# Optimization experiments

Hardware: AMD Instinct MI355X
Metric: run time of the kernel (lower is better)

The kernel has to match this reference:

```python
import jax, jax.numpy as jnp
import numpy as np

DIM = 1536; NH = 12; HD = DIM // NH; C = HD // 2  # C = 64
F, H, W = 12, 16, 16; S = F * H * W  # 3072 tokens
NFPB = 3       # num_frame_per_block (block-causal granularity)
LOCAL = 6      # local_attn_size in frames
SINK = 1       # sink_size in frames
EPS = 1e-06


def setup_inputs():
    key = jax.random.key(0)
    ks = jax.random.split(key, 6)
    sc = 1.0 / np.sqrt(DIM)
    x = jax.random.normal(ks[0], (1, S, DIM), jnp.float32)
    Wq = jax.random.normal(ks[1], (DIM, DIM), jnp.float32) * sc
    Wk = jax.random.normal(ks[2], (DIM, DIM), jnp.float32) * sc
    Wv = jax.random.normal(ks[3], (DIM, DIM), jnp.float32) * sc
    Wo = jax.random.normal(ks[4], (DIM, DIM), jnp.float32) * sc
    zeros = jnp.zeros((DIM,), jnp.float32); ones = jnp.ones((DIM,), jnp.float32)
    # RoPE table: unit-modulus complex freqs stored as cos/sin, shape [1024, C]
    ang = jax.random.uniform(ks[5], (1024, C), jnp.float32) * (2.0 * np.pi)
    return dict(x=x, Wq=Wq, bq=zeros, Wk=Wk, bk=zeros, Wv=Wv, bv=zeros,
                Wo=Wo, bo=zeros, gq=ones, gk=ones,
                freqs_cos=jnp.cos(ang), freqs_sin=jnp.sin(ang), f=F, h=H, w=W)


def _rms_norm(x, g):
    y = x * jax.lax.rsqrt(jnp.mean(x * x, axis=-1, keepdims=True) + EPS)
    return y * g


def _pos_table(tab, f, h, w):
    # split [1024, C] into frame/height/width parts and broadcast to [f*h*w, C]
    cf = C - 2 * (C // 3); ch = C // 3
    tf = jnp.broadcast_to(tab[:f, :cf][:, None, None, :], (f, h, w, cf))
    th = jnp.broadcast_to(tab[:h, cf:cf + ch][None, :, None, :], (f, h, w, ch))
    tw = jnp.broadcast_to(tab[:w, cf + ch:][None, None, :, :], (f, h, w, ch))
    return jnp.concatenate([tf, th, tw], axis=-1).reshape(f * h * w, C)


def _rope(x, cosp, sinp):
    # complex multiply on consecutive (real, imag) pairs along head_dim
    b, s, n, d = x.shape
    xp = x.reshape(b, s, n, d // 2, 2)
    xr, xi = xp[..., 0], xp[..., 1]
    cp = cosp[None, :, None, :]; sp = sinp[None, :, None, :]
    out = jnp.stack([xr * cp - xi * sp, xr * sp + xi * cp], axis=-1)
    return out.reshape(b, s, n, d)


def reference(x, Wq, bq, Wk, bk, Wv, bv, Wo, bo, gq, gk, freqs_cos, freqs_sin, f, h, w):
    b, s, _ = x.shape
    q = _rms_norm(x @ Wq.T + bq, gq).reshape(b, s, NH, HD)
    k = _rms_norm(x @ Wk.T + bk, gk).reshape(b, s, NH, HD)
    v = (x @ Wv.T + bv).reshape(b, s, NH, HD)
    cosp = _pos_table(freqs_cos, f, h, w)
    sinp = _pos_table(freqs_sin, f, h, w)
    rq = _rope(q, cosp, sinp)
    rk = _rope(k, cosp, sinp)
    # block mask: block-causal (bidirectional inside a frame-block) + local window + sink
    idx = jnp.arange(s)
    frame = idx // (h * w)
    blk = frame // NFPB
    qb, kb = blk[:, None], blk[None, :]
    mask = (kb <= qb) & ((((qb - kb) * NFPB) < LOCAL) | (frame[None, :] < SINK))
    scores = jnp.einsum('bqnd,bknd->bnqk', rq, rk) * (HD ** -0.5)
    scores = jnp.where(mask[None, None], scores, jnp.finfo(scores.dtype).min)
    probs = jax.nn.softmax(scores, axis=-1)
    out = jnp.einsum('bnqk,bknd->bqnd', probs, v).reshape(b, s, DIM)
    return out @ Wo.T + bo
```

## Files before the change

kernel.cpp:

```cpp
#include <hip/hip_runtime.h>
#include <stdint.h>

typedef unsigned short u16;
typedef __attribute__((ext_vector_type(8))) short bf16x8;
typedef __attribute__((ext_vector_type(4))) short bf16x4;
typedef __attribute__((ext_vector_type(4))) float f32x4;

constexpr int DMODEL = 1536;
constexpr int SEQ    = 3072;
constexpr int NHEAD  = 12;
constexpr int HDIM   = 128;

__device__ __forceinline__ u16 f2bf(float f){
  union { float f; unsigned u; } v; v.f = f;
  return (u16)((v.u + 0x7fffu + ((v.u >> 16) & 1u)) >> 16);
}

__global__ __launch_bounds__(256) void cvt_all(
    const float* __restrict__ x,  const float* __restrict__ wq,
    const float* __restrict__ wk, const float* __restrict__ wv, const float* __restrict__ wo,
    u16* __restrict__ xb, u16* __restrict__ wqb, u16* __restrict__ wkb,
    u16* __restrict__ wvb, u16* __restrict__ wob)
{
  const int NX = (SEQ * DMODEL) / 4;
  const int NW = (DMODEL * DMODEL) / 4;
  int i = blockIdx.x * 256 + threadIdx.x;
  const float* src; u16* dst; int off;
  if      (i < NX)          { src = x;  dst = xb;  off = i; }
  else if (i < NX + NW)     { src = wq; dst = wqb; off = i - NX; }
  else if (i < NX + 2 * NW) { src = wk; dst = wkb; off = i - NX - NW; }
  else if (i < NX + 3 * NW) { src = wv; dst = wvb; off = i - NX - 2 * NW; }
  else                      { src = wo; dst = wob; off = i - NX - 3 * NW; }
  float4 f = ((const float4*)src)[off];
  ushort4 o;
  o.x = f2bf(f.x); o.y = f2bf(f.y); o.z = f2bf(f.z); o.w = f2bf(f.w);
  ((ushort4*)dst)[off] = o;
}

__device__ __forceinline__ void gload16(const u16* g, u16* l){
  __builtin_amdgcn_global_load_lds((const __attribute__((address_space(1))) void*)g,
                                   (__attribute__((address_space(3))) void*)l, 16, 0, 0);
}

__global__ __launch_bounds__(512, 2) void gemm_qkv256(const u16* __restrict__ xb,
    const u16* __restrict__ wqb, const u16* __restrict__ wkb, const u16* __restrict__ wvb,
    const float* __restrict__ bq, const float* __restrict__ bk, const float* __restrict__ bv,
    float* __restrict__ qf, float* __restrict__ kf, u16* __restrict__ vt)
{
  __shared__ u16 lds[2][2][16384];

  const int tid  = threadIdx.x;
  const int lane = tid & 63;
  const int wid  = tid >> 6;
  const int wm   = wid >> 2;
  const int wn   = wid & 3;
  const int l15  = lane & 15, lg = lane >> 4;
  const int swz  = (l15 & 7) << 4;

  const int bid  = blockIdx.x;
  const int sbid = (bid & 7) * 27 + (bid >> 3);
  const int mt   = sbid / 18, nt = sbid % 18;
  const int sel  = nt / 6, ntl = nt % 6;
  const u16* W = sel == 0 ? wqb : (sel == 1 ? wkb : wvb);
  const float* bias = sel == 0 ? bq : (sel == 1 ? bk : bv);
  const int m0 = mt * 256, n0 = ntl * 256;

  const char* Ag = (const char*)(xb + (size_t)m0 * DMODEL);
  const char* Bg = (const char*)(W  + (size_t)n0 * DMODEL);

  auto stage_op = [&](int buf, int op, const char* G, int kt){
#pragma unroll
    for (int c = 0; c < 4; c++){
      int ob  = c * 8192 + wid * 1024 + lane * 16;
      int row = ob >> 7, colb = ob & 127;
      gload16((const u16*)(G + (size_t)row * (DMODEL * 2) + (size_t)kt * 128
                             + (colb ^ ((row & 7) << 4))),
              (u16*)((char*)&lds[buf][op][0] + c * 8192 + wid * 1024));
    }
  };

  f32x4 acc[8][4];
#pragma unroll
  for (int i = 0; i < 8; i++)
#pragma unroll
    for (int j = 0; j < 4; j++){ f32x4 z = {0.f,0.f,0.f,0.f}; acc[i][j] = z; }

  const int NK = DMODEL / 64;

  stage_op(0, 0, Ag, 0);
  stage_op(0, 1, Bg, 0);
  asm volatile("s_waitcnt vmcnt(0)" ::: "memory");
  __builtin_amdgcn_sched_barrier(0);
  __builtin_amdgcn_s_barrier();
  __builtin_amdgcn_sched_barrier(0);

#pragma unroll 1
  for (int t = 0; t < NK; t++){
    const int b = t & 1;
    const char* Abase = (const char*)&lds[b][0][0];
    const char* Bbase = (const char*)&lds[b][1][0];
    bf16x8 bfr[4][2], afr[2][2];

#pragma unroll
    for (int ni = 0; ni < 4; ni++){
      int rb = wn * 64 + ni * 16 + l15;
#pragma unroll
      for (int ks = 0; ks < 2; ks++)
        bfr[ni][ks] = *(const bf16x8*)(Bbase + rb * 128 + ((ks * 64 + lg * 16) ^ swz));
    }
#pragma unroll
    for (int i = 0; i < 2; i++){
      int ra = wm * 128 + i * 16 + l15;
#pragma unroll
      for (int ks = 0; ks < 2; ks++)
        afr[i][ks] = *(const bf16x8*)(Abase + ra * 128 + ((ks * 64 + lg * 16) ^ swz));
    }
    if (t + 1 < NK) stage_op(b ^ 1, 0, Ag, t + 1);
    __builtin_amdgcn_sched_barrier(0);
    __builtin_amdgcn_s_barrier();
    __builtin_amdgcn_sched_barrier(0);
    __builtin_amdgcn_s_setprio(1);
#pragma unroll
    for (int i = 0; i < 2; i++)
#pragma unroll
      for (int ni = 0; ni < 4; ni++)
#pragma unroll
        for (int ks = 0; ks < 2; ks++)
          acc[i][ni] = __builtin_amdgcn_mfma_f32_16x16x32_bf16(afr[i][ks], bfr[ni][ks], acc[i][ni], 0, 0, 0);
    __builtin_amdgcn_s_setprio(0);
    __builtin_amdgcn_sched_barrier(0);
    __builtin_amdgcn_s_barrier();
    __builtin_amdgcn_sched_barrier(0);

#pragma unroll
    for (int qd = 1; qd < 4; qd++){
#pragma unroll
      for (int i = 0; i < 2; i++){
        int ra = wm * 128 + (qd * 2 + i) * 16 + l15;
#pragma unroll
        for (int ks = 0; ks < 2; ks++)
          afr[i][ks] = *(const bf16x8*)(Abase + ra * 128 + ((ks * 64 + lg * 16) ^ swz));
      }
      if (qd == 1 && t + 1 < NK) stage_op(b ^ 1, 1, Bg, t + 1);
      __builtin_amdgcn_sched_barrier(0);
      __builtin_amdgcn_s_barrier();
      __builtin_amdgcn_sched_barrier(0);
      __builtin_amdgcn_s_setprio(1);
#pragma unroll
      for (int i = 0; i < 2; i++)
#pragma unroll
        for (int ni = 0; ni < 4; ni++)
#pragma unroll
          for (int ks = 0; ks < 2; ks++)
            acc[qd * 2 + i][ni] = __builtin_amdgcn_mfma_f32_16x16x32_bf16(afr[i][ks], bfr[ni][ks], acc[qd * 2 + i][ni], 0, 0, 0);
      __builtin_amdgcn_s_setprio(0);
      if (qd == 3) asm volatile("s_waitcnt vmcnt(0)" ::: "memory");
      __builtin_amdgcn_sched_barrier(0);
      __builtin_amdgcn_s_barrier();
      __builtin_amdgcn_sched_barrier(0);
    }
  }

  if (sel != 2){
    float* C = sel == 0 ? qf : kf;
#pragma unroll
    for (int mi = 0; mi < 8; mi++){
      int row = m0 + wm * 128 + mi * 16 + lg * 4;
#pragma unroll
      for (int ni = 0; ni < 4; ni++){
        int col = n0 + wn * 64 + ni * 16 + l15;
        float bvv = bias[col];
#pragma unroll
        for (int r = 0; r < 4; r++)
          C[(size_t)(row + r) * DMODEL + col] = acc[mi][ni][r] + bvv;
      }
    }
  } else {
#pragma unroll
    for (int mi = 0; mi < 8; mi++){
      int gbase = m0 + wm * 128 + (mi >> 1) * 32 + lg * 8 + (mi & 1) * 4;
#pragma unroll
      for (int ni = 0; ni < 4; ni++){
        int d = n0 + wn * 64 + ni * 16 + l15;
        float bvv = bias[d];
        ushort4 o;
        o.x = f2bf(acc[mi][ni][0] + bvv);
        o.y = f2bf(acc[mi][ni][1] + bvv);
        o.z = f2bf(acc[mi][ni][2] + bvv);
        o.w = f2bf(acc[mi][ni][3] + bvv);
        *(ushort4*)(vt + (size_t)d * SEQ + gbase) = o;
      }
    }
  }
}

__device__ __forceinline__ void gemm_core(const u16* __restrict__ A, const u16* __restrict__ W,
    const float* __restrict__ bias, float* __restrict__ C, int m0, int n0,
    u16* As, u16* Bs)
{
  const int tid  = threadIdx.x;
  const int lane = tid & 63;
  const int wv   = tid >> 6;
  const int wm   = wv & 1, wn = wv >> 1;
  const int l15  = lane & 15, lg = lane >> 4;

  f32x4 acc[4][4];
#pragma unroll
  for (int i = 0; i < 4; i++)
#pragma unroll
    for (int j = 0; j < 4; j++){ f32x4 z = {0.f,0.f,0.f,0.f}; acc[i][j] = z; }

  const int r0 = wv * 16 + (lane >> 2);
  const int r1 = (wv + 4) * 16 + (lane >> 2);
  const int cc = (lane & 3) * 8;
  const u16* Ab = A + (size_t)m0 * DMODEL;
  const u16* Wb = W + (size_t)n0 * DMODEL;

  auto stageg = [&](int b, int k0){
    gload16(Ab + (size_t)r0 * DMODEL + k0 + cc, As + b * 4096 + wv * 512);
    gload16(Ab + (size_t)r1 * DMODEL + k0 + cc, As + b * 4096 + (wv + 4) * 512);
    gload16(Wb + (size_t)r0 * DMODEL + k0 + cc, Bs + b * 4096 + wv * 512);
    gload16(Wb + (size_t)r1 * DMODEL + k0 + cc, Bs + b * 4096 + (wv + 4) * 512);
  };

  stageg(0, 0);
  __syncthreads();

  for (int k0 = 0; k0 < DMODEL; k0 += 32){
    int b = (k0 >> 5) & 1;
    if (k0 + 32 < DMODEL) stageg(b ^ 1, k0 + 32);

    const u16* Ar = As + b * 4096;
    const u16* Br = Bs + b * 4096;
    bf16x8 af[4], bfr[4];
#pragma unroll
    for (int mi = 0; mi < 4; mi++)
      af[mi]  = *(const bf16x8*)(Ar + (wm * 64 + mi * 16 + l15) * 32 + lg * 8);
#pragma unroll
    for (int ni = 0; ni < 4; ni++)
      bfr[ni] = *(const bf16x8*)(Br + (wn * 64 + ni * 16 + l15) * 32 + lg * 8);
#pragma unroll
    for (int mi = 0; mi < 4; mi++)
#pragma unroll
      for (int ni = 0; ni < 4; ni++)
        acc[mi][ni] = __builtin_amdgcn_mfma_f32_16x16x32_bf16(af[mi], bfr[ni], acc[mi][ni], 0, 0, 0);
    __syncthreads();
  }

#pragma unroll
  for (int mi = 0; mi < 4; mi++){
    int row = m0 + wm * 64 + mi * 16 + (lg << 2);
#pragma unroll
    for (int ni = 0; ni < 4; ni++){
      int col = n0 + wn * 64 + ni * 16 + l15;
      float bvv = bias[col];
#pragma unroll
      for (int r = 0; r < 4; r++)
        C[(size_t)(row + r) * DMODEL + col] = acc[mi][ni][r] + bvv;
    }
  }
}

__global__ __launch_bounds__(256) void gemm_o(const u16* __restrict__ ab,
    const u16* __restrict__ wob, const float* __restrict__ bo, float* __restrict__ out)
{
  __shared__ u16 As[2 * 4096], Bs[2 * 4096];
  gemm_core(ab, wob, bo, out, blockIdx.x * 128, blockIdx.y * 128, As, Bs);
}

__global__ __launch_bounds__(256) void rmsrope_kernel(
    const float* __restrict__ qin, const float* __restrict__ kin,
    const float* __restrict__ gq, const float* __restrict__ gk,
    const float* __restrict__ fcos, const float* __restrict__ fsin,
    u16* __restrict__ rq, u16* __restrict__ rk)
{
  int gw   = (blockIdx.x * 256 + threadIdx.x) >> 6;
  int lane = threadIdx.x & 63;
  int s    = gw >> 1;
  int pass = gw & 1;
  const float* in = pass ? kin : qin;
  const float* g  = pass ? gk  : gq;
  u16* outp       = pass ? rk  : rq;

  const float* row = in + (size_t)s * DMODEL + lane * 24;
  float v[24];
#pragma unroll
  for (int j = 0; j < 6; j++) *(float4*)(v + 4 * j) = ((const float4*)row)[j];

  float ss = 0.f;
#pragma unroll
  for (int j = 0; j < 24; j++) ss += v[j] * v[j];
#pragma unroll
  for (int m = 1; m < 64; m <<= 1) ss += __shfl_xor(ss, m);
  float scale = rsqrtf(ss * (1.0f / (float)DMODEL) + 1e-6f);

  float gv[24];
  const float* gp = g + lane * 24;
#pragma unroll
  for (int j = 0; j < 6; j++) *(float4*)(gv + 4 * j) = ((const float4*)gp)[j];

  int fi = s >> 8, hi2 = (s >> 4) & 15, wi = s & 15;
  u16 o[24];
#pragma unroll
  for (int jp = 0; jp < 12; jp++){
    int i  = lane * 12 + jp;
    int pi = i & 63;
    int idx = pi < 22 ? fi : (pi < 43 ? hi2 : wi);
    float cv = fcos[idx * 64 + pi];
    float sv = fsin[idx * 64 + pi];
    float xr = v[2 * jp]     * scale * gv[2 * jp];
    float xi = v[2 * jp + 1] * scale * gv[2 * jp + 1];
    o[2 * jp]     = f2bf(xr * cv - xi * sv);
    o[2 * jp + 1] = f2bf(xr * sv + xi * cv);
  }
  u16* op = outp + (size_t)s * DMODEL + lane * 24;
#pragma unroll
  for (int j = 0; j < 3; j++) *(bf16x8*)(op + 8 * j) = *(bf16x8*)(o + 8 * j);
}

__global__ __launch_bounds__(256, 2) void attn_kernel(const u16* __restrict__ rq,
    const u16* __restrict__ rk, const u16* __restrict__ vt,
    float* __restrict__ pO, float* __restrict__ pl)
{
  __shared__ u16 Ks[2][8192];
  __shared__ u16 Vs[2][8192];

  const int tid  = threadIdx.x;
  const int lane = tid & 63;
  const int wv   = tid >> 6;
  const int head = blockIdx.y;
  const int bid  = blockIdx.x;
  int qb, blk, sub;
  if      (bid < 24){ qb = 3; blk = bid >> 1;        sub = bid & 1; }
  else if (bid < 48){ qb = 2; blk = (bid - 24) >> 1; sub = bid & 1; }
  else if (bid < 72){ qb = 1; blk = (bid - 48) >> 1; sub = bid & 1; }
  else              { qb = 0; blk = bid - 72;        sub = 0; }
  const int qblk = qb * 12 + blk;
  const int q0   = qblk * 64 + wv * 16;
  const int l15  = lane & 15, lg = lane >> 4;
  const int swz  = (l15 & 7) << 4;
  const float sc = 0.08838834764831845f;

  int r1s = 0, r1e = 0, r0e = 0;
  if      (qb == 0){ r0e = 768; }
  else if (qb == 1){ r0e = 1536; }
  else if (qb == 2){ r0e = 256; r1s = 768;  r1e = 2304; }
  else             { r0e = 256; r1s = 1536; r1e = 3072; }
  const int nt0 = r0e >> 6;
  const int nt  = nt0 + ((r1e - r1s) >> 6);
  const int hl  = (qb == 0) ? nt : (nt >> 1);
  const int ts  = sub * hl, te = ts + hl;

  const char* rkB = (const char*)rk;
  const char* vtB = (const char*)vt;
  auto k0_of = [&](int t){ return t < nt0 ? t * 64 : (r1s + (t - nt0) * 64); };

  auto stage = [&](int buf, int k0){
    char* Kd = (char*)Ks[buf];
    char* Vd = (char*)Vs[buf];
#pragma unroll
    for (int c = 0; c < 4; c++){
      int o = c * 4096 + wv * 1024 + lane * 16;
      int row = o >> 8, colb = o & 255;
      gload16((const u16*)(rkB + (size_t)(k0 + row) * (DMODEL * 2) + head * (HDIM * 2)
                               + (colb ^ ((row & 7) << 4))),
              (u16*)(Kd + c * 4096 + wv * 1024));
    }
#pragma unroll
    for (int c = 0; c < 4; c++){
      int o = c * 4096 + wv * 1024 + lane * 16;
      int row = o >> 7, colb = o & 127;
      gload16((const u16*)(vtB + (size_t)(head * HDIM + row) * (SEQ * 2) + (size_t)k0 * 2
                               + (colb ^ ((row & 7) << 4))),
              (u16*)(Vd + c * 4096 + wv * 1024));
    }
  };

  bf16x8 qfr[4];
  const u16* qbase = rq + (size_t)(q0 + l15) * DMODEL + head * HDIM + lg * 8;
#pragma unroll
  for (int c = 0; c < 4; c++) qfr[c] = *(const bf16x8*)(qbase + c * 32);

  f32x4 oacc[8];
#pragma unroll
  for (int i = 0; i < 8; i++){ f32x4 z = {0.f,0.f,0.f,0.f}; oacc[i] = z; }
  float l_run = 0.f;

  stage(0, k0_of(ts));
  __syncthreads();

  for (int t = ts; t < te; t++){
    int buf = (t - ts) & 1;
    if (t + 1 < te) stage(buf ^ 1, k0_of(t + 1));

    const char* Kb = (const char*)Ks[buf];
    const char* Vb = (const char*)Vs[buf];
#pragma unroll
    for (int half = 0; half < 2; half++){
      const int kt = half * 32;
      const char* kr0 = Kb + (kt + l15) * 256;
      const char* kr1 = kr0 + 16 * 256;
      bf16x8 kf0[4], kf1[4];
#pragma unroll
      for (int c = 0; c < 4; c++){
        kf0[c] = *(const bf16x8*)(kr0 + ((lg * 16 + c * 64) ^ swz));
        kf1[c] = *(const bf16x8*)(kr1 + ((lg * 16 + c * 64) ^ swz));
      }
      f32x4 s0 = {0.f,0.f,0.f,0.f}, s1 = {0.f,0.f,0.f,0.f};
      __builtin_amdgcn_s_setprio(1);
#pragma unroll
      for (int c = 0; c < 4; c++){
        s0 = __builtin_amdgcn_mfma_f32_16x16x32_bf16(kf0[c], qfr[c], s0, 0, 0, 0);
        s1 = __builtin_amdgcn_mfma_f32_16x16x32_bf16(kf1[c], qfr[c], s1, 0, 0, 0);
      }
      __builtin_amdgcn_s_setprio(0);

      bf16x8 pf;
      float lsum = 0.f;
#pragma unroll
      for (int r = 0; r < 4; r++){
        float e0 = __expf(fmaf(s0[r], sc, -12.f));
        float e1 = __expf(fmaf(s1[r], sc, -12.f));
        lsum += e0 + e1;
        pf[r]     = (short)f2bf(e0);
        pf[r + 4] = (short)f2bf(e1);
      }
      l_run += lsum;

      __builtin_amdgcn_s_setprio(1);
#pragma unroll
      for (int ch = 0; ch < 8; ch++){
        bf16x8 vf8 = *(const bf16x8*)(Vb + (ch * 16 + l15) * 128 + ((half * 64 + lg * 16) ^ swz));
        oacc[ch] = __builtin_amdgcn_mfma_f32_16x16x32_bf16(pf, vf8, oacc[ch], 0, 0, 0);
      }
      __builtin_amdgcn_s_setprio(0);
    }
    __syncthreads();
  }

  const size_t punit = (size_t)(head * 84 + bid);
  l_run += __shfl_xor(l_run, 16);
  l_run += __shfl_xor(l_run, 32);
  if (lg == 0) pl[punit * 64 + wv * 16 + l15] = l_run;

  float* po = pO + punit * 8192;
#pragma unroll
  for (int ch = 0; ch < 8; ch++)
#pragma unroll
    for (int r = 0; r < 4; r++)
      po[(wv * 16 + lg * 4 + r) * 128 + ch * 16 + l15] = oacc[ch][r];
}

__global__ __launch_bounds__(256) void attn_reduce(const float* __restrict__ pO,
    const float* __restrict__ pl, u16* __restrict__ ao)
{
  const int qblk = blockIdx.x;
  const int head = blockIdx.y;
  const int qb = qblk / 12, blk = qblk % 12;
  int b0, nu;
  if      (qb == 0){ b0 = 72 + blk;     nu = 1; }
  else if (qb == 1){ b0 = 48 + 2 * blk; nu = 2; }
  else if (qb == 2){ b0 = 24 + 2 * blk; nu = 2; }
  else             { b0 = 2 * blk;      nu = 2; }
  const size_t u0 = (size_t)(head * 84 + b0);
  const float* O0 = pO + u0 * 8192;
  const float* L0 = pl + u0 * 64;

  __shared__ float ls[64];
  int t = threadIdx.x;
  if (t < 64) ls[t] = L0[t] + (nu == 2 ? L0[64 + t] : 0.f);
  __syncthreads();

  int q = t >> 2, dc = (t & 3) * 32;
  float inv = 1.f / ls[q];
  const float* a0 = O0 + q * 128 + dc;
  const float* a1 = a0 + 8192;
  u16 buf[32];
#pragma unroll
  for (int j = 0; j < 32; j += 4){
    float4 xv = *(const float4*)(a0 + j);
    if (nu == 2){
      float4 y = *(const float4*)(a1 + j);
      xv.x += y.x; xv.y += y.y; xv.z += y.z; xv.w += y.w;
    }
    buf[j]     = f2bf(xv.x * inv);
    buf[j + 1] = f2bf(xv.y * inv);
    buf[j + 2] = f2bf(xv.z * inv);
    buf[j + 3] = f2bf(xv.w * inv);
  }
  u16* op = ao + (size_t)(qblk * 64 + q) * DMODEL + head * HDIM + dc;
#pragma unroll
  for (int j = 0; j < 32; j += 8) *(bf16x8*)(op + j) = *(bf16x8*)(buf + j);
}

extern "C" void kernel_launch(void* const* d_in, const int* in_sizes, int n_in,
                              void* d_out, int out_size, void* d_ws, size_t ws_size,
                              hipStream_t stream)
{
  const float* x    = (const float*)d_in[0];
  const float* Wq   = (const float*)d_in[1];
  const float* bq   = (const float*)d_in[2];
  const float* Wk   = (const float*)d_in[3];
  const float* bk   = (const float*)d_in[4];
  const float* Wv   = (const float*)d_in[5];
  const float* bv   = (const float*)d_in[6];
  const float* Wo   = (const float*)d_in[7];
  const float* bo   = (const float*)d_in[8];
  const float* gq   = (const float*)d_in[9];
  const float* gk   = (const float*)d_in[10];
  const float* fcos = (const float*)d_in[11];
  const float* fsin = (const float*)d_in[12];
  float* out = (float*)d_out;

  char* ws = (char*)d_ws;
  size_t off = 0;
  auto alloc = [&](size_t bytes){
    void* p = ws + off;
    off += (bytes + 255) & ~(size_t)255;
    return p;
  };
  const size_t SD = (size_t)SEQ * DMODEL;
  const size_t WW = (size_t)DMODEL * DMODEL;
  u16*   xb  = (u16*)  alloc(SD * 2);
  u16*   wqb = (u16*)  alloc(WW * 2);
  u16*   wkb = (u16*)  alloc(WW * 2);
  u16*   wvb = (u16*)  alloc(WW * 2);
  u16*   wob = (u16*)  alloc(WW * 2);
  float* qf  = (float*)alloc(SD * 4);
  float* kf  = (float*)alloc(SD * 4);
  u16*   rq  = (u16*)  alloc(SD * 2);
  u16*   rk  = (u16*)  alloc(SD * 2);
  u16*   vt  = (u16*)  alloc(SD * 2);
  u16*   ao  = (u16*)  alloc(SD * 2);
  float* pl  = (float*)alloc((size_t)1008 * 64 * 4);
  float* pO  = qf;

  const int NX = (SEQ * DMODEL) / 4, NW = (DMODEL * DMODEL) / 4;
  cvt_all<<<(NX + 4 * NW) / 256, 256, 0, stream>>>(x, Wq, Wk, Wv, Wo, xb, wqb, wkb, wvb, wob);
  gemm_qkv256<<<216, 512, 0, stream>>>(xb, wqb, wkb, wvb, bq, bk, bv, qf, kf, vt);
  rmsrope_kernel<<<(SEQ * 2) / 4, 256, 0, stream>>>(qf, kf, gq, gk, fcos, fsin, rq, rk);
  attn_kernel<<<dim3(84, NHEAD), 256, 0, stream>>>(rq, rk, vt, pO, pl);
  attn_reduce<<<dim3(48, NHEAD), 256, 0, stream>>>(pO, pl, ao);
  gemm_o<<<dim3(SEQ / 128, DMODEL / 128), 256, 0, stream>>>(ao, wob, bo, out);
}
```

Before: 289.9 us.

## Double attention query tile to 128 rows and remap blocks for XCD locality

Each attention workgroup now handles 128 query rows instead of 64, with every wave processing two 16-row query groups that share the same K/V fragments loaded from shared memory. This halves K/V global and LDS traffic per query row. The 1D grid is remapped with a stride-8 interleave so that blocks of the same head land on the same XCD. The reduce kernel and partial-buffer layout are adjusted to match. The cost is more registers per thread (doubled accumulators) and fewer workgroups (504 vs 1008), which may reduce occupancy and load balance.

```diff
diff --git a/kernel.cpp b/kernel.cpp
--- a/kernel.cpp
+++ b/kernel.cpp
@@ -328,15 +328,17 @@
   const int tid  = threadIdx.x;
   const int lane = tid & 63;
   const int wv   = tid >> 6;
-  const int head = blockIdx.y;
-  const int bid  = blockIdx.x;
+  const int lin  = blockIdx.x;
+  const int u    = (lin & 7) * 63 + (lin >> 3);
+  const int head = u / 42;
+  const int bid  = u % 42;
   int qb, blk, sub;
-  if      (bid < 24){ qb = 3; blk = bid >> 1;        sub = bid & 1; }
-  else if (bid < 48){ qb = 2; blk = (bid - 24) >> 1; sub = bid & 1; }
-  else if (bid < 72){ qb = 1; blk = (bid - 48) >> 1; sub = bid & 1; }
-  else              { qb = 0; blk = bid - 72;        sub = 0; }
-  const int qblk = qb * 12 + blk;
-  const int q0   = qblk * 64 + wv * 16;
+  if      (bid < 12){ qb = 3; blk = bid >> 1;        sub = bid & 1; }
+  else if (bid < 24){ qb = 2; blk = (bid - 12) >> 1; sub = bid & 1; }
+  else if (bid < 36){ qb = 1; blk = (bid - 24) >> 1; sub = bid & 1; }
+  else              { qb = 0; blk = bid - 36;        sub = 0; }
+  const int qblk = qb * 6 + blk;
+  const int q0   = qblk * 128 + wv * 32;
   const int l15  = lane & 15, lg = lane >> 4;
   const int swz  = (l15 & 7) << 4;
   const float sc = 0.08838834764831845f;
@@ -376,15 +378,20 @@
     }
   };
 
-  bf16x8 qfr[4];
-  const u16* qbase = rq + (size_t)(q0 + l15) * DMODEL + head * HDIM + lg * 8;
-#pragma unroll
-  for (int c = 0; c < 4; c++) qfr[c] = *(const bf16x8*)(qbase + c * 32);
-
-  f32x4 oacc[8];
-#pragma unroll
-  for (int i = 0; i < 8; i++){ f32x4 z = {0.f,0.f,0.f,0.f}; oacc[i] = z; }
-  float l_run = 0.f;
+  bf16x8 qfr[2][4];
+#pragma unroll
+  for (int qg = 0; qg < 2; qg++){
+    const u16* qbase = rq + (size_t)(q0 + qg * 16 + l15) * DMODEL + head * HDIM + lg * 8;
+#pragma unroll
+    for (int c = 0; c < 4; c++) qfr[qg][c] = *(const bf16x8*)(qbase + c * 32);
+  }
+
+  f32x4 oacc[2][8];
+#pragma unroll
+  for (int qg = 0; qg < 2; qg++)
+#pragma unroll
+    for (int i = 0; i < 8; i++){ f32x4 z = {0.f,0.f,0.f,0.f}; oacc[qg][i] = z; }
+  float l_run[2] = {0.f, 0.f};
 
   stage(0, k0_of(ts));
   __syncthreads();
@@ -406,49 +413,64 @@
         kf0[c] = *(const bf16x8*)(kr0 + ((lg * 16 + c * 64) ^ swz));
         kf1[c] = *(const bf16x8*)(kr1 + ((lg * 16 + c * 64) ^ swz));
       }
-      f32x4 s0 = {0.f,0.f,0.f,0.f}, s1 = {0.f,0.f,0.f,0.f};
+      f32x4 s0[2], s1[2];
+#pragma unroll
+      for (int qg = 0; qg < 2; qg++){ f32x4 z = {0.f,0.f,0.f,0.f}; s0[qg] = z; s1[qg] = z; }
       __builtin_amdgcn_s_setprio(1);
 #pragma unroll
-      for (int c = 0; c < 4; c++){
-        s0 = __builtin_amdgcn_mfma_f32_16x16x32_bf16(kf0[c], qfr[c], s0, 0, 0, 0);
-        s1 = __builtin_amdgcn_mfma_f32_16x16x32_bf16(kf1[c], qfr[c], s1, 0, 0, 0);
+      for (int c = 0; c < 4; c++)
+#pragma unroll
+        for (int qg = 0; qg < 2; qg++){
+          s0[qg] = __builtin_amdgcn_mfma_f32_16x16x32_bf16(kf0[c], qfr[qg][c], s0[qg], 0, 0, 0);
+          s1[qg] = __builtin_amdgcn_mfma_f32_16x16x32_bf16(kf1[c], qfr[qg][c], s1[qg], 0, 0, 0);
+        }
+      __builtin_amdgcn_s_setprio(0);
+
+      bf16x8 pf[2];
+#pragma unroll
+      for (int qg = 0; qg < 2; qg++){
+        float lsum = 0.f;
+#pragma unroll
+        for (int r = 0; r < 4; r++){
+          float e0 = __expf(fmaf(s0[qg][r], sc, -12.f));
+          float e1 = __expf(fmaf(s1[qg][r], sc, -12.f));
+          lsum += e0 + e1;
+          pf[qg][r]     = (short)f2bf(e0);
+          pf[qg][r + 4] = (short)f2bf(e1);
+        }
+        l_run[qg] += lsum;
+      }
+
+      __builtin_amdgcn_s_setprio(1);
+#pragma unroll
+      for (int ch = 0; ch < 8; ch++){
+        bf16x8 vf8 = *(const bf16x8*)(Vb + (ch * 16 + l15) * 128 + ((half * 64 + lg * 16) ^ swz));
+#pragma unroll
+        for (int qg = 0; qg < 2; qg++)
+          oacc[qg][ch] = __builtin_amdgcn_mfma_f32_16x16x32_bf16(pf[qg], vf8, oacc[qg][ch], 0, 0, 0);
       }
       __builtin_amdgcn_s_setprio(0);
-
-      bf16x8 pf;
-      float lsum = 0.f;
-#pragma unroll
-      for (int r = 0; r < 4; r++){
-        float e0 = __expf(fmaf(s0[r], sc, -12.f));
-        float e1 = __expf(fmaf(s1[r], sc, -12.f));
-        lsum += e0 + e1;
-        pf[r]     = (short)f2bf(e0);
-        pf[r + 4] = (short)f2bf(e1);
-      }
-      l_run += lsum;
-
-      __builtin_amdgcn_s_setprio(1);
-#pragma unroll
-      for (int ch = 0; ch < 8; ch++){
-        bf16x8 vf8 = *(const bf16x8*)(Vb + (ch * 16 + l15) * 128 + ((half * 64 + lg * 16) ^ swz));
-        oacc[ch] = __builtin_amdgcn_mfma_f32_16x16x32_bf16(pf, vf8, oacc[ch], 0, 0, 0);
-      }
-      __builtin_amdgcn_s_setprio(0);
     }
     __syncthreads();
   }
 
-  const size_t punit = (size_t)(head * 84 + bid);
-  l_run += __shfl_xor(l_run, 16);
-  l_run += __shfl_xor(l_run, 32);
-  if (lg == 0) pl[punit * 64 + wv * 16 + l15] = l_run;
-
-  float* po = pO + punit * 8192;
-#pragma unroll
-  for (int ch = 0; ch < 8; ch++)
-#pragma unroll
-    for (int r = 0; r < 4; r++)
-      po[(wv * 16 + lg * 4 + r) * 128 + ch * 16 + l15] = oacc[ch][r];
+  const size_t punit = (size_t)(head * 42 + bid);
+#pragma unroll
+  for (int qg = 0; qg < 2; qg++){
+    float lr = l_run[qg];
+    lr += __shfl_xor(lr, 16);
+    lr += __shfl_xor(lr, 32);
+    if (lg == 0) pl[punit * 128 + wv * 32 + qg * 16 + l15] = lr;
+  }
+
+  float* po = pO + punit * 16384;
+#pragma unroll
+  for (int qg = 0; qg < 2; qg++)
+#pragma unroll
+    for (int ch = 0; ch < 8; ch++)
+#pragma unroll
+      for (int r = 0; r < 4; r++)
+        po[(wv * 32 + qg * 16 + lg * 4 + r) * 128 + ch * 16 + l15] = oacc[qg][ch][r];
 }
 
 __global__ __launch_bounds__(256) void attn_reduce(const float* __restrict__ pO,
@@ -456,28 +478,28 @@
 {
   const int qblk = blockIdx.x;
   const int head = blockIdx.y;
-  const int qb = qblk / 12, blk = qblk % 12;
+  const int qb = qblk / 6, blk = qblk % 6;
   int b0, nu;
-  if      (qb == 0){ b0 = 72 + blk;     nu = 1; }
-  else if (qb == 1){ b0 = 48 + 2 * blk; nu = 2; }
-  else if (qb == 2){ b0 = 24 + 2 * blk; nu = 2; }
+  if      (qb == 0){ b0 = 36 + blk;     nu = 1; }
+  else if (qb == 1){ b0 = 24 + 2 * blk; nu = 2; }
+  else if (qb == 2){ b0 = 12 + 2 * blk; nu = 2; }
   else             { b0 = 2 * blk;      nu = 2; }
-  const size_t u0 = (size_t)(head * 84 + b0);
-  const float* O0 = pO + u0 * 8192;
-  const float* L0 = pl + u0 * 64;
-
-  __shared__ float ls[64];
+  const size_t u0 = (size_t)(head * 42 + b0);
+  const float* O0 = pO + u0 * 16384;
+  const float* L0 = pl + u0 * 128;
+
+  __shared__ float ls[128];
   int t = threadIdx.x;
-  if (t < 64) ls[t] = L0[t] + (nu == 2 ? L0[64 + t] : 0.f);
+  if (t < 128) ls[t] = L0[t] + (nu == 2 ? L0[128 + t] : 0.f);
   __syncthreads();
 
-  int q = t >> 2, dc = (t & 3) * 32;
+  int q = t >> 1, dc = (t & 1) * 64;
   float inv = 1.f / ls[q];
   const float* a0 = O0 + q * 128 + dc;
-  const float* a1 = a0 + 8192;
-  u16 buf[32];
-#pragma unroll
-  for (int j = 0; j < 32; j += 4){
+  const float* a1 = a0 + 16384;
+  u16 buf[64];
+#pragma unroll
+  for (int j = 0; j < 64; j += 4){
     float4 xv = *(const float4*)(a0 + j);
     if (nu == 2){
       float4 y = *(const float4*)(a1 + j);
@@ -488,9 +510,9 @@
     buf[j + 2] = f2bf(xv.z * inv);
     buf[j + 3] = f2bf(xv.w * inv);
   }
-  u16* op = ao + (size_t)(qblk * 64 + q) * DMODEL + head * HDIM + dc;
-#pragma unroll
-  for (int j = 0; j < 32; j += 8) *(bf16x8*)(op + j) = *(bf16x8*)(buf + j);
+  u16* op = ao + (size_t)(qblk * 128 + q) * DMODEL + head * HDIM + dc;
+#pragma unroll
+  for (int j = 0; j < 64; j += 8) *(bf16x8*)(op + j) = *(bf16x8*)(buf + j);
 }
 
 extern "C" void kernel_launch(void* const* d_in, const int* in_sizes, int n_in,
@@ -532,14 +554,14 @@
   u16*   rk  = (u16*)  alloc(SD * 2);
   u16*   vt  = (u16*)  alloc(SD * 2);
   u16*   ao  = (u16*)  alloc(SD * 2);
-  float* pl  = (float*)alloc((size_t)1008 * 64 * 4);
+  float* pl  = (float*)alloc((size_t)504 * 128 * 4);
   float* pO  = qf;
 
   const int NX = (SEQ * DMODEL) / 4, NW = (DMODEL * DMODEL) / 4;
   cvt_all<<<(NX + 4 * NW) / 256, 256, 0, stream>>>(x, Wq, Wk, Wv, Wo, xb, wqb, wkb, wvb, wob);
   gemm_qkv256<<<216, 512, 0, stream>>>(xb, wqb, wkb, wvb, bq, bk, bv, qf, kf, vt);
   rmsrope_kernel<<<(SEQ * 2) / 4, 256, 0, stream>>>(qf, kf, gq, gk, fcos, fsin, rq, rk);
-  attn_kernel<<<dim3(84, NHEAD), 256, 0, stream>>>(rq, rk, vt, pO, pl);
-  attn_reduce<<<dim3(48, NHEAD), 256, 0, stream>>>(pO, pl, ao);
+  attn_kernel<<<504, 256, 0, stream>>>(rq, rk, vt, pO, pl);
+  attn_reduce<<<dim3(24, NHEAD), 256, 0, stream>>>(pO, pl, ao);
   gemm_o<<<dim3(SEQ / 128, DMODEL / 128), 256, 0, stream>>>(ao, wob, bo, out);
 }
```

After: 280.6 us. -3.2%, faster.
